# Kernel optimization log

Measured on AMD Instinct MI355X. Metric: run time of the kernel, lower is better.

Reference implementation:

```python
import jax, jax.numpy as jnp
import numpy as np

EPS = 1e-5


def _gcn_conv(x, src, dst, norm, W, b, n_nodes):
    # PyG GCNConv: transform, then normalized scatter-add aggregation (self-loops included in src/dst)
    h = x @ W                                   # [N, out]
    msg = h[src] * norm[:, None]                # gather over edges [E+N, out]
    agg = jax.ops.segment_sum(msg, dst, num_segments=n_nodes)
    return agg + b


def _bn(x, gamma, beta):
    # BatchNorm1d in training mode: batch stats over node axis, biased variance
    mu = jnp.mean(x, axis=0)
    var = jnp.mean((x - mu) ** 2, axis=0)
    return (x - mu) * jax.lax.rsqrt(var + EPS) * gamma + beta


def setup_inputs() -> dict:
    key = jax.random.key(0)
    ks = jax.random.split(key, 8)
    N, E, F_in, H, F_out = 50000, 800000, 32, 96, 2
    x = jax.random.normal(ks[0], (N, F_in), dtype=jnp.float32)
    edge_index = jax.random.randint(ks[1], (2, E), 0, N, dtype=jnp.int64)
    def lin(k, fi, fo):
        s = 1.0 / np.sqrt(fi)
        return jax.random.uniform(k, (fi, fo), jnp.float32, -s, s)
    W1 = lin(ks[2], F_in, H); b1 = jnp.zeros((H,), jnp.float32)
    W2 = lin(ks[3], H, H);    b2 = jnp.zeros((H,), jnp.float32)
    W3 = lin(ks[4], H, H);    b3 = jnp.zeros((H,), jnp.float32)
    W4 = lin(ks[5], H, F_out); b4 = jnp.zeros((F_out,), jnp.float32)
    g1 = jnp.ones((H,), jnp.float32); be1 = jnp.zeros((H,), jnp.float32)
    g2 = jnp.ones((H,), jnp.float32); be2 = jnp.zeros((H,), jnp.float32)
    g3 = jnp.ones((H,), jnp.float32); be3 = jnp.zeros((H,), jnp.float32)
    return dict(x=x, edge_index=edge_index,
                W1=W1, b1=b1, g1=g1, be1=be1,
                W2=W2, b2=b2, g2=g2, be2=be2,
                W3=W3, b3=b3, g3=g3, be3=be3,
                W4=W4, b4=b4)


def reference(x, edge_index, W1, b1, g1, be1, W2, b2, g2, be2, W3, b3, g3, be3, W4, b4):
    N = x.shape[0]
    loop = jnp.arange(N, dtype=edge_index.dtype)
    src = jnp.concatenate([edge_index[0], loop])   # add self-loops
    dst = jnp.concatenate([edge_index[1], loop])
    deg = jax.ops.segment_sum(jnp.ones_like(dst, dtype=x.dtype), dst, num_segments=N)
    dinv = jnp.where(deg > 0, jax.lax.rsqrt(deg), 0.0)
    norm = dinv[src] * dinv[dst]                   # D^{-1/2} (A+I) D^{-1/2}

    h = jax.nn.relu(_bn(_gcn_conv(x, src, dst, norm, W1, b1, N), g1, be1))
    h = jax.nn.relu(_bn(_gcn_conv(h, src, dst, norm, W2, b2, N), g2, be2))
    h = jax.nn.relu(_bn(_gcn_conv(h, src, dst, norm, W3, b3, N), g3, be3))
    return _gcn_conv(h, src, dst, norm, W4, b4, N)
```

## Files before the change

kernel.cpp:

```cpp
#include <hip/hip_runtime.h>
#include <hip/hip_bf16.h>

using bf16x8 = __attribute__((ext_vector_type(8))) short;
using f32x4  = __attribute__((ext_vector_type(4))) float;

#define FS_CHUNK 4096

__device__ __forceinline__ float ldf(const void* p, size_t i, float isf){
  if (isf > 0.5f) return ((const float*)p)[i];
  unsigned int u = ((unsigned int)((const unsigned short*)p)[i]) << 16;
  return __uint_as_float(u);
}
__device__ __forceinline__ unsigned short f2bf(float v){
  unsigned int u = __float_as_uint(v);
  u = (u + 0x7FFFu + ((u >> 16) & 1u)) >> 16;
  return (unsigned short)u;
}
__device__ __forceinline__ unsigned int pk2(float a, float b){
  return (unsigned int)f2bf(a) | ((unsigned int)f2bf(b) << 16);
}
__device__ __forceinline__ float lo16(unsigned int u){ return __uint_as_float(u << 16); }
__device__ __forceinline__ float hi16(unsigned int u){ return __uint_as_float(u & 0xFFFF0000u); }

__global__ void k_fill(unsigned short* o, unsigned short v, int n){
  int i = blockIdx.x*blockDim.x + threadIdx.x;
  if (i < n) o[i] = v;
}

__global__ void k_prep(const unsigned short* xh, const unsigned int* eu,
                       float* flag, int nelemX, long long E,
                       const void* W1, const void* W2, const void* W3, const void* W4,
                       unsigned short* __restrict__ Wt1, unsigned short* __restrict__ Wt2,
                       unsigned short* __restrict__ Wt3, float* __restrict__ W4f,
                       int* __restrict__ cnt, float* __restrict__ stAll, int n){
  int t = threadIdx.x;
  if (blockIdx.x > 0){
    int total = n + 4609;
    for (int i = (int)(blockIdx.x-1)*256 + t; i < total; i += (int)(gridDim.x-1)*256){
      if (i < n) cnt[i] = 0; else stAll[i - n] = 0.f;
    }
    return;
  }
  __shared__ int sf32, si64;
  __shared__ float sisf;
  if (t == 0){ sf32 = 0; si64 = 1; }
  __syncthreads();
  {
    int i = 2*t;
    if (i < nelemX){
      unsigned e8 = (xh[i] >> 7) & 0xFFu;
      if (e8 >= 140u) sf32 = 1;
    }
    if ((long long)(2*t + 1) < 2*E){
      if (eu[2*t + 1] != 0u) si64 = 0;
    }
  }
  __syncthreads();
  if (t == 0){
    flag[0] = (float)sf32; flag[1] = (float)si64;
    sisf = (float)sf32;
  }
  __syncthreads();
  float isf = sisf;
  for (int q = t; q < 3072; q += 256){
    int nn = q >> 5, k = q & 31;
    Wt1[q] = f2bf(ldf(W1, (size_t)96*k + nn, isf));
  }
  for (int q = t; q < 9216; q += 256){
    int nn = q/96, k = q - 96*nn;
    Wt2[q] = f2bf(ldf(W2, (size_t)96*k + nn, isf));
    Wt3[q] = f2bf(ldf(W3, (size_t)96*k + nn, isf));
  }
  if (t < 192) W4f[t] = ldf(W4, t, isf);
}

__global__ void k_cnt2(const int* __restrict__ ei, const float* __restrict__ flag,
                       int* __restrict__ cnt, int* __restrict__ ec,
                       long long E, int n){
  long long i = (long long)blockIdx.x*blockDim.x + threadIdx.x;
  long long i0 = 2*i;
  if (i0 >= E) return;
  bool i64 = (flag[1] > 0.5f);
  bool two = (i0 + 1 < E);
  int s0, d0, s1 = 0, d1 = -1;
  if ((E & 1LL) == 0){
    if (i64){
      uint4 vs = ((const uint4*)ei)[i];
      uint4 vd = ((const uint4*)(ei + 2*E))[i];
      s0 = (int)vs.x; s1 = (int)vs.z; d0 = (int)vd.x; d1 = (int)vd.z;
    } else {
      int2 vs = ((const int2*)ei)[i];
      int2 vd = ((const int2*)(ei + E))[i];
      s0 = vs.x; s1 = vs.y; d0 = vd.x; d1 = vd.y;
    }
  } else {
    if (i64){ s0 = ei[2*i0]; d0 = ei[2*E + 2*i0];
              if (two){ s1 = ei[2*i0+2]; d1 = ei[2*E + 2*i0 + 2]; } }
    else    { s0 = ei[i0];   d0 = ei[E + i0];
              if (two){ s1 = ei[i0+1];   d1 = ei[E + i0 + 1]; } }
  }
  bool ok0 = ((unsigned)s0 < (unsigned)n) && ((unsigned)d0 < (unsigned)n);
  bool ok1 = two && ((unsigned)s1 < (unsigned)n) && ((unsigned)d1 < (unsigned)n);
  if (!ok0){ s0 = -1; d0 = -1; }
  if (!ok1){ s1 = -1; d1 = -1; }
  if (two){
    int4 o; o.x = s0; o.y = d0; o.z = s1; o.w = d1;
    ((int4*)ec)[i] = o;
  } else {
    int2 o; o.x = s0; o.y = d0;
    ((int2*)ec)[i0] = o;
  }
  if (ok0) atomicAdd(&cnt[d0], 1);
  if (ok1) atomicAdd(&cnt[d1], 1);
}

__global__ void k_emit2(const int* __restrict__ cnt, int* __restrict__ gctr,
                        int* __restrict__ rowst, int* __restrict__ cursor,
                        float* __restrict__ dinv, int n){
  int i = blockIdx.x*256 + threadIdx.x;
  int lane = threadIdx.x & 63;
  int v = (i < n) ? cnt[i] : 0;
  int s = v;
  #pragma unroll
  for (int off = 1; off < 64; off <<= 1){
    int u = __shfl_up(s, off, 64);
    if (lane >= off) s += u;
  }
  int wtot = __shfl(s, 63, 64);
  int base = 0;
  if (lane == 63) base = atomicAdd(gctr, wtot);
  base = __shfl(base, 63, 64);
  if (i < n){
    int r = base + s - v;
    rowst[i]  = r;
    cursor[i] = r;
    dinv[i]   = rsqrtf((float)(1 + v));
  }
}

template<typename IT>
__global__ __launch_bounds__(256) void k_fx(const int* __restrict__ ec,
      int* __restrict__ cursor, IT* __restrict__ csr,
      long long E, int n, int gF8,
      const void* __restrict__ x, const float* __restrict__ flag,
      const float* __restrict__ dinv, unsigned short* __restrict__ XS){
  int t = threadIdx.x;
  if ((int)blockIdx.x < gF8){
    int part = blockIdx.x & 7;
    long long base = (long long)(blockIdx.x >> 3) * FS_CHUNK;
    int pl = (int)(((long long)n *  part     ) >> 3);
    int pr = (int)(((long long)n * (part + 1)) >> 3);
    long long lim = base + FS_CHUNK < E ? base + FS_CHUNK : E;
    for (long long i = base + 2*t; i < lim; i += 512){
      int4 v = ((const int4*)ec)[i >> 1];
      if (v.y >= pl && v.y < pr && (unsigned)v.x < (unsigned)n){
        int p = atomicAdd(&cursor[v.y], 1);
        csr[p] = (IT)v.x;
      }
      if (i + 1 < lim && v.w >= pl && v.w < pr && (unsigned)v.z < (unsigned)n){
        int p = atomicAdd(&cursor[v.w], 1);
        csr[p] = (IT)v.z;
      }
    }
    return;
  }
  int q = (int)(blockIdx.x - gF8)*256 + t;
  if (q < 4*n){
    int node = q >> 2, part = q & 3;
    float isf = flag[0];
    float di = dinv[node];
    uint4 o;
    if (isf > 0.5f){
      const float* xr = (const float*)x + (size_t)32*node + 8*part;
      o.x = pk2(xr[0]*di, xr[1]*di); o.y = pk2(xr[2]*di, xr[3]*di);
      o.z = pk2(xr[4]*di, xr[5]*di); o.w = pk2(xr[6]*di, xr[7]*di);
    } else {
      uint4 v = ((const uint4*)x)[(size_t)4*node + part];
      o.x = pk2(lo16(v.x)*di, hi16(v.x)*di);
      o.y = pk2(lo16(v.y)*di, hi16(v.y)*di);
      o.z = pk2(lo16(v.z)*di, hi16(v.z)*di);
      o.w = pk2(lo16(v.w)*di, hi16(v.w)*di);
    }
    ((uint4*)XS)[q] = o;
  }
}

#define ACC8(v) { a0+=lo16((v).x); a1+=hi16((v).x); a2+=lo16((v).y); a3+=hi16((v).y); \
                  a4+=lo16((v).z); a5+=hi16((v).z); a6+=lo16((v).w); a7+=hi16((v).w); }

template<typename IT>
__global__ __launch_bounds__(256) void k_aggx(const uint4* __restrict__ xs4,
      const int* __restrict__ rowst, const int* __restrict__ cnt,
      const IT* __restrict__ csr, const float* __restrict__ dinv,
      const unsigned short* __restrict__ Wt1b,
      unsigned short* __restrict__ Zb, float* __restrict__ stout, int n){
  __shared__ __align__(16) unsigned short Xs[64][40];
  __shared__ __align__(16) unsigned short Wt[96][40];
  __shared__ float bs[96], bq[96];
  int t = threadIdx.x;
  for (int q = t; q < 384; q += 256){
    uint4 v = ((const uint4*)Wt1b)[q];
    *(uint4*)&Wt[q >> 2][(q & 3)*8] = v;
  }
  if (t < 96){ bs[t] = 0.f; bq[t] = 0.f; }
  int g = t & 3, ty = t >> 2;
  int node = blockIdx.x*64 + ty;
  float a0=0.f,a1=0.f,a2=0.f,a3=0.f,a4=0.f,a5=0.f,a6=0.f,a7=0.f;
  if (node < n){
    uint4 v = xs4[(size_t)node*4 + g];
    ACC8(v);
    int b = rowst[node], e = b + cnt[node];
    int j = b;
    for (; j + 7 < e; j += 8){
      uint4 v0 = xs4[(size_t)csr[j]  *4 + g];
      uint4 v1 = xs4[(size_t)csr[j+1]*4 + g];
      uint4 v2 = xs4[(size_t)csr[j+2]*4 + g];
      uint4 v3 = xs4[(size_t)csr[j+3]*4 + g];
      uint4 v4 = xs4[(size_t)csr[j+4]*4 + g];
      uint4 v5 = xs4[(size_t)csr[j+5]*4 + g];
      uint4 v6 = xs4[(size_t)csr[j+6]*4 + g];
      uint4 v7 = xs4[(size_t)csr[j+7]*4 + g];
      ACC8(v0); ACC8(v1); ACC8(v2); ACC8(v3);
      ACC8(v4); ACC8(v5); ACC8(v6); ACC8(v7);
    }
    for (; j + 3 < e; j += 4){
      uint4 v0 = xs4[(size_t)csr[j]  *4 + g];
      uint4 v1 = xs4[(size_t)csr[j+1]*4 + g];
      uint4 v2 = xs4[(size_t)csr[j+2]*4 + g];
      uint4 v3 = xs4[(size_t)csr[j+3]*4 + g];
      ACC8(v0); ACC8(v1); ACC8(v2); ACC8(v3);
    }
    for (; j < e; ++j){
      uint4 vv = xs4[(size_t)csr[j]*4 + g];
      ACC8(vv);
    }
    float di = dinv[node];
    a0*=di; a1*=di; a2*=di; a3*=di; a4*=di; a5*=di; a6*=di; a7*=di;
  }
  uint4 o;
  o.x = pk2(a0,a1); o.y = pk2(a2,a3); o.z = pk2(a4,a5); o.w = pk2(a6,a7);
  *(uint4*)&Xs[ty][8*g] = o;
  __syncthreads();
  int wv = t >> 6, lane = t & 63;
  int m = lane & 15, quad = lane >> 4;
  bf16x8 av = *(const bf16x8*)&Xs[16*wv + m][8*quad];
  f32x4 acc[6];
  #pragma unroll
  for (int c = 0; c < 6; ++c) acc[c] = (f32x4)(0.f);
  #pragma unroll
  for (int c = 0; c < 6; ++c){
    bf16x8 bv = *(const bf16x8*)&Wt[16*c + m][8*quad];
    acc[c] = __builtin_amdgcn_mfma_f32_16x16x32_bf16(av, bv, acc[c], 0, 0, 0);
  }
  int rowbase = blockIdx.x*64 + 16*wv + 4*quad;
  #pragma unroll
  for (int c = 0; c < 6; ++c){
    int col = 16*c + m;
    float s = 0.f, q = 0.f;
    #pragma unroll
    for (int r = 0; r < 4; ++r){
      int rr = rowbase + r;
      if (rr < n){
        unsigned short h = f2bf(acc[c][r]);
        Zb[(size_t)96*rr + col] = h;
        float br = __uint_as_float(((unsigned int)h) << 16);
        s += br; q += br*br;
      }
    }
    atomicAdd(&bs[col], s);
    atomicAdd(&bq[col], q);
  }
  __syncthreads();
  if (t < 96){
    int rep = blockIdx.x & 7;
    atomicAdd(&stout[192*rep + t],      bs[t]);
    atomicAdd(&stout[192*rep + 96 + t], bq[t]);
  }
}

template<typename IT>
__global__ __launch_bounds__(192) void k_agg(const uint4* __restrict__ hsr,
      const int* __restrict__ rowst, const int* __restrict__ cnt,
      const IT* __restrict__ csr,
      const float* __restrict__ dinv, uint4* __restrict__ zb4,
      float* __restrict__ stout, int n){
  __shared__ float ls[16][97], lq[16][97];
  int g = threadIdx.x, ty = threadIdx.y;
  int t = ty*12 + g;
  int node = blockIdx.x*16 + ty;
  float r[8];
  if (node < n){
    uint4 v = hsr[(size_t)node*12 + g];
    float a0 = lo16(v.x), a1 = hi16(v.x), a2 = lo16(v.y), a3 = hi16(v.y);
    float a4 = lo16(v.z), a5 = hi16(v.z), a6 = lo16(v.w), a7 = hi16(v.w);
    int b = rowst[node], e = b + cnt[node];
    int j = b;
    for (; j + 7 < e; j += 8){
      uint4 v0 = hsr[(size_t)csr[j]  *12 + g];
      uint4 v1 = hsr[(size_t)csr[j+1]*12 + g];
      uint4 v2 = hsr[(size_t)csr[j+2]*12 + g];
      uint4 v3 = hsr[(size_t)csr[j+3]*12 + g];
      uint4 v4 = hsr[(size_t)csr[j+4]*12 + g];
      uint4 v5 = hsr[(size_t)csr[j+5]*12 + g];
      uint4 v6 = hsr[(size_t)csr[j+6]*12 + g];
      uint4 v7 = hsr[(size_t)csr[j+7]*12 + g];
      ACC8(v0); ACC8(v1); ACC8(v2); ACC8(v3);
      ACC8(v4); ACC8(v5); ACC8(v6); ACC8(v7);
    }
    for (; j + 3 < e; j += 4){
      uint4 v0 = hsr[(size_t)csr[j]  *12 + g];
      uint4 v1 = hsr[(size_t)csr[j+1]*12 + g];
      uint4 v2 = hsr[(size_t)csr[j+2]*12 + g];
      uint4 v3 = hsr[(size_t)csr[j+3]*12 + g];
      ACC8(v0); ACC8(v1); ACC8(v2); ACC8(v3);
    }
    for (; j < e; ++j){
      uint4 vv = hsr[(size_t)csr[j]*12 + g];
      ACC8(vv);
    }
    float di = dinv[node];
    uint4 o;
    o.x = pk2(a0*di, a1*di);
    o.y = pk2(a2*di, a3*di);
    o.z = pk2(a4*di, a5*di);
    o.w = pk2(a6*di, a7*di);
    zb4[(size_t)node*12 + g] = o;
    r[0]=lo16(o.x); r[1]=hi16(o.x); r[2]=lo16(o.y); r[3]=hi16(o.y);
    r[4]=lo16(o.z); r[5]=hi16(o.z); r[6]=lo16(o.w); r[7]=hi16(o.w);
  } else {
    #pragma unroll
    for (int jj = 0; jj < 8; ++jj) r[jj] = 0.f;
  }
  #pragma unroll
  for (int jj = 0; jj < 8; ++jj){
    ls[ty][8*g + jj] = r[jj];
    lq[ty][8*g + jj] = r[jj]*r[jj];
  }
  __syncthreads();
  if (t < 96){
    float s = 0.f, q = 0.f;
    #pragma unroll
    for (int rr = 0; rr < 16; ++rr){ s += ls[rr][t]; q += lq[rr][t]; }
    int rep = blockIdx.x & 7;
    atomicAdd(&stout[192*rep + t],      s);
    atomicAdd(&stout[192*rep + 96 + t], q);
  }
}

__global__ __launch_bounds__(256) void k_linm(const unsigned short* __restrict__ zb,
      const unsigned short* __restrict__ Wtb, const float* __restrict__ st,
      const void* __restrict__ gam, const void* __restrict__ bet,
      const float* __restrict__ flag, const float* __restrict__ dinv,
      unsigned short* __restrict__ HS, int n, float invN){
  __shared__ float sa[96], sc[96];
  __shared__ __align__(16) unsigned short Ys[64][104];
  __shared__ __align__(16) unsigned short Wt[96][104];
  int t = threadIdx.x;
  if (t < 96){
    float ssum = 0.f, qsum = 0.f;
    #pragma unroll
    for (int r = 0; r < 8; ++r){ ssum += st[192*r + t]; qsum += st[192*r + 96 + t]; }
    float isf = flag[0];
    float mu  = ssum*invN;
    float var = fmaxf(qsum*invN - mu*mu, 0.f);
    float istd = rsqrtf(var + 1e-5f);
    float a = ldf(gam, t, isf)*istd;
    sa[t] = a; sc[t] = ldf(bet, t, isf) - mu*a;
  }
  for (int q = t; q < 1152; q += 256){
    uint4 v = ((const uint4*)Wtb)[q];
    *(uint4*)&Wt[q/12][8*(q - 12*(q/12))] = v;
  }
  __syncthreads();
  {
    int row = t >> 2, part = t & 3;
    int node = blockIdx.x*64 + row;
    if (node < n){
      const uint4* zr = (const uint4*)(zb + (size_t)96*node) + 3*part;
      #pragma unroll
      for (int q = 0; q < 3; ++q){
        uint4 zz = zr[q];
        int k = 24*part + 8*q;
        float y0 = fmaxf(lo16(zz.x)*sa[k]   + sc[k],   0.f);
        float y1 = fmaxf(hi16(zz.x)*sa[k+1] + sc[k+1], 0.f);
        float y2 = fmaxf(lo16(zz.y)*sa[k+2] + sc[k+2], 0.f);
        float y3 = fmaxf(hi16(zz.y)*sa[k+3] + sc[k+3], 0.f);
        float y4 = fmaxf(lo16(zz.z)*sa[k+4] + sc[k+4], 0.f);
        float y5 = fmaxf(hi16(zz.z)*sa[k+5] + sc[k+5], 0.f);
        float y6 = fmaxf(lo16(zz.w)*sa[k+6] + sc[k+6], 0.f);
        float y7 = fmaxf(hi16(zz.w)*sa[k+7] + sc[k+7], 0.f);
        *(unsigned int*)&Ys[row][k]     = pk2(y0, y1);
        *(unsigned int*)&Ys[row][k + 2] = pk2(y2, y3);
        *(unsigned int*)&Ys[row][k + 4] = pk2(y4, y5);
        *(unsigned int*)&Ys[row][k + 6] = pk2(y6, y7);
      }
    } else {
      unsigned int* yp = (unsigned int*)&Ys[row][24*part];
      #pragma unroll
      for (int q = 0; q < 12; ++q) yp[q] = 0u;
    }
  }
  __syncthreads();
  int wv = t >> 6, lane = t & 63;
  int m = lane & 15, quad = lane >> 4;
  bf16x8 av[3];
  #pragma unroll
  for (int kt = 0; kt < 3; ++kt)
    av[kt] = *(const bf16x8*)&Ys[16*wv + m][32*kt + 8*quad];
  f32x4 acc[6];
  #pragma unroll
  for (int c = 0; c < 6; ++c) acc[c] = (f32x4)(0.f);
  #pragma unroll
  for (int c = 0; c < 6; ++c){
    const unsigned short* wrow = &Wt[16*c + m][8*quad];
    #pragma unroll
    for (int kt = 0; kt < 3; ++kt){
      bf16x8 bv = *(const bf16x8*)(wrow + 32*kt);
      acc[c] = __builtin_amdgcn_mfma_f32_16x16x32_bf16(av[kt], bv, acc[c], 0, 0, 0);
    }
  }
  int rowbase = blockIdx.x*64 + 16*wv + 4*quad;
  float div[4];
  #pragma unroll
  for (int r = 0; r < 4; ++r){ int rr = rowbase + r; div[r] = (rr < n) ? dinv[rr] : 0.f; }
  #pragma unroll
  for (int c = 0; c < 6; ++c){
    int col = 16*c + m;
    #pragma unroll
    for (int r = 0; r < 4; ++r){
      int rr = rowbase + r;
      if (rr < n) HS[(size_t)96*rr + col] = f2bf(acc[c][r]*div[r]);
    }
  }
}

__global__ __launch_bounds__(256) void k_lin4(const unsigned short* __restrict__ zb,
      const float* __restrict__ Wf, const float* __restrict__ st,
      const void* __restrict__ gam, const void* __restrict__ bet,
      const float* __restrict__ flag, const float* __restrict__ dinv,
      float* __restrict__ hs2, int n, float invN){
  __shared__ float sa[96], sc[96];
  int t = threadIdx.x;
  if (t < 96){
    float ssum = 0.f, qsum = 0.f;
    #pragma unroll
    for (int r = 0; r < 8; ++r){ ssum += st[192*r + t]; qsum += st[192*r + 96 + t]; }
    float isf = flag[0];
    float mu  = ssum*invN;
    float var = fmaxf(qsum*invN - mu*mu, 0.f);
    float istd = rsqrtf(var + 1e-5f);
    float a = ldf(gam, t, isf)*istd;
    sa[t] = a; sc[t] = ldf(bet, t, isf) - mu*a;
  }
  __syncthreads();
  int i = blockIdx.x*blockDim.x + t;
  if (i >= n) return;
  const uint4* zr = (const uint4*)(zb + (size_t)96*i);
  float a0 = 0.f, a1 = 0.f;
  #pragma unroll
  for (int q = 0; q < 12; ++q){
    uint4 zz = zr[q];
    int k = 8*q;
    float y;
    y = fmaxf(lo16(zz.x)*sa[k]   + sc[k],   0.f); a0 += y*Wf[2*k];    a1 += y*Wf[2*k+1];
    y = fmaxf(hi16(zz.x)*sa[k+1] + sc[k+1], 0.f); a0 += y*Wf[2*k+2];  a1 += y*Wf[2*k+3];
    y = fmaxf(lo16(zz.y)*sa[k+2] + sc[k+2], 0.f); a0 += y*Wf[2*k+4];  a1 += y*Wf[2*k+5];
    y = fmaxf(hi16(zz.y)*sa[k+3] + sc[k+3], 0.f); a0 += y*Wf[2*k+6];  a1 += y*Wf[2*k+7];
    y = fmaxf(lo16(zz.z)*sa[k+4] + sc[k+4], 0.f); a0 += y*Wf[2*k+8];  a1 += y*Wf[2*k+9];
    y = fmaxf(hi16(zz.z)*sa[k+5] + sc[k+5], 0.f); a0 += y*Wf[2*k+10]; a1 += y*Wf[2*k+11];
    y = fmaxf(lo16(zz.w)*sa[k+6] + sc[k+6], 0.f); a0 += y*Wf[2*k+12]; a1 += y*Wf[2*k+13];
    y = fmaxf(hi16(zz.w)*sa[k+7] + sc[k+7], 0.f); a0 += y*Wf[2*k+14]; a1 += y*Wf[2*k+15];
  }
  float di = dinv[i];
  hs2[(size_t)2*i]   = di*a0;
  hs2[(size_t)2*i+1] = di*a1;
}

template<typename IT>
__global__ void k_agg2(const float2* __restrict__ hs2, const int* __restrict__ rowst,
                       const int* __restrict__ cnt, const IT* __restrict__ csr,
                       const float* __restrict__ dinv,
                       const void* __restrict__ b4, const float* __restrict__ flag,
                       void* __restrict__ out, int n){
  int node = blockIdx.x*blockDim.x + threadIdx.x;
  if (node >= n) return;
  float2 a = hs2[node];
  int b = rowst[node], e = b + cnt[node];
  int j = b;
  for (; j + 3 < e; j += 4){
    float2 v0 = hs2[(size_t)csr[j]];
    float2 v1 = hs2[(size_t)csr[j+1]];
    float2 v2 = hs2[(size_t)csr[j+2]];
    float2 v3 = hs2[(size_t)csr[j+3]];
    a.x += v0.x + v1.x + v2.x + v3.x;
    a.y += v0.y + v1.y + v2.y + v3.y;
  }
  for (; j < e; ++j){
    float2 v = hs2[(size_t)csr[j]];
    a.x += v.x; a.y += v.y;
  }
  float isf = flag[0];
  float di = dinv[node];
  float v0 = a.x*di + ldf(b4, 0, isf);
  float v1 = a.y*di + ldf(b4, 1, isf);
  if (isf > 0.5f){
    ((float*)out)[(size_t)2*node]   = v0;
    ((float*)out)[(size_t)2*node+1] = v1;
  } else {
    ((unsigned short*)out)[(size_t)2*node]   = f2bf(v0);
    ((unsigned short*)out)[(size_t)2*node+1] = f2bf(v1);
  }
}

extern "C" void kernel_launch(void* const* d_in, const int* in_sizes, int n_in,
                              void* d_out, int out_size, void* d_ws, size_t ws_size,
                              hipStream_t stream)
{
  const int B = 256;
  unsigned short* outh = (unsigned short*)d_out;

  if (n_in < 16){
    k_fill<<<(out_size+B-1)/B, B, 0, stream>>>(outh, 0x3F40u, out_size); return;
  }
  const int N = in_sizes[0] / 32;
  const long long E = in_sizes[1] / 2;
  if (in_sizes[0] % 32 != 0 || out_size != 2*N){
    k_fill<<<(out_size+B-1)/B, B, 0, stream>>>(outh, 0x3F60u, out_size); return;
  }
  const bool u16 = (N < 65536);

  size_t Npad = ((size_t)N + 3) & ~(size_t)3;
  float* ws   = (float*)d_ws;
  float* dinv = ws;
  float* hs2  = dinv + Npad;
  float* flag = hs2 + (size_t)2*N;
  float* stAll= flag + 4;
  float* W4f  = stAll + 4612;
  unsigned short* Wt1b = (unsigned short*)(W4f + 192);
  unsigned short* Wt2b = Wt1b + 3072;
  unsigned short* Wt3b = Wt2b + 9216;
  int* cnt    = (int*)(Wt3b + 9216);
  int* cursor = cnt + N;
  int* rowst  = cursor + N;
  void* csrv  = (void*)(rowst + N);
  size_t csrBytes = (size_t)E * (u16 ? 2 : 4);
  uintptr_t hp_ = (uintptr_t)csrv + csrBytes;
  hp_ = (hp_ + 15) & ~(uintptr_t)15;
  unsigned short* HS = (unsigned short*)hp_;
  unsigned short* Zb = HS + (size_t)96*N;
  int* ec = (int*)(Zb + (size_t)96*N);

  size_t needB = ((uintptr_t)(ec + 2*E + 4) - (uintptr_t)d_ws) + 64;
  if (ws_size < needB){
    k_fill<<<(out_size+B-1)/B, B, 0, stream>>>(outh, 0x3F00u, out_size); return;
  }

  unsigned short* XS = HS;

  const void* x  = d_in[0];
  const int*  ei = (const int*)d_in[1];
  const void* W1 = d_in[2];
  const void* g1 = d_in[4];  const void* be1 = d_in[5];
  const void* W2 = d_in[6];
  const void* g2 = d_in[8];  const void* be2 = d_in[9];
  const void* W3 = d_in[10];
  const void* g3 = d_in[12]; const void* be3 = d_in[13];
  const void* W4 = d_in[14];
  const void* b4 = d_in[15];

  float* stA = stAll;
  float* stB = stAll + 1536;
  float* stC = stAll + 3072;
  int*   gctr = (int*)(stAll + 4608);

  int gN  = (N + B - 1)/B;
  long long hE = (E + 1)/2;
  int gE2 = (int)((hE + B - 1)/B); if (gE2 < 1) gE2 = 1;
  int nb  = (N + 255)/256;
  int gA  = (N + 15)/16;
  int gL  = (N + 63)/64;
  int gXS = (4*N + 255)/256;
  int gF8 = (int)((E + FS_CHUNK - 1)/FS_CHUNK) * 8;
  float invN = 1.0f / (float)N;
  dim3 ablk(12,16);

  k_prep<<<33, B, 0, stream>>>((const unsigned short*)x, (const unsigned int*)ei,
                               flag, in_sizes[0], E, W1, W2, W3, W4,
                               Wt1b, Wt2b, Wt3b, W4f, cnt, stAll, N);
  k_cnt2<<<gE2, B, 0, stream>>>(ei, flag, cnt, ec, E, N);
  k_emit2<<<nb, B, 0, stream>>>(cnt, gctr, rowst, cursor, dinv, N);

  if (u16){
    unsigned short* csr = (unsigned short*)csrv;
    k_fx<unsigned short><<<gF8 + gXS, B, 0, stream>>>(ec, cursor, csr, E, N, gF8,
                                                      x, flag, dinv, XS);
    k_aggx<unsigned short><<<gL, B, 0, stream>>>((const uint4*)XS, rowst, cnt, csr, dinv, Wt1b, Zb, stA, N);
    k_linm<<<gL, B, 0, stream>>>(Zb, Wt2b, stA, g1, be1, flag, dinv, HS, N, invN);
    k_agg<unsigned short><<<gA, ablk, 0, stream>>>((const uint4*)HS, rowst, cnt, csr, dinv, (uint4*)Zb, stB, N);
    k_linm<<<gL, B, 0, stream>>>(Zb, Wt3b, stB, g2, be2, flag, dinv, HS, N, invN);
    k_agg<unsigned short><<<gA, ablk, 0, stream>>>((const uint4*)HS, rowst, cnt, csr, dinv, (uint4*)Zb, stC, N);
    k_lin4<<<gN, B, 0, stream>>>(Zb, W4f, stC, g3, be3, flag, dinv, hs2, N, invN);
    k_agg2<unsigned short><<<gN, B, 0, stream>>>((const float2*)hs2, rowst, cnt, csr, dinv, b4, flag, d_out, N);
  } else {
    int* csr = (int*)csrv;
    k_fx<int><<<gF8 + gXS, B, 0, stream>>>(ec, cursor, csr, E, N, gF8,
                                           x, flag, dinv, XS);
    k_aggx<int><<<gL, B, 0, stream>>>((const uint4*)XS, rowst, cnt, csr, dinv, Wt1b, Zb, stA, N);
    k_linm<<<gL, B, 0, stream>>>(Zb, Wt2b, stA, g1, be1, flag, dinv, HS, N, invN);
    k_agg<int><<<gA, ablk, 0, stream>>>((const uint4*)HS, rowst, cnt, csr, dinv, (uint4*)Zb, stB, N);
    k_linm<<<gL, B, 0, stream>>>(Zb, Wt3b, stB, g2, be2, flag, dinv, HS, N, invN);
    k_agg<int><<<gA, ablk, 0, stream>>>((const uint4*)HS, rowst, cnt, csr, dinv, (uint4*)Zb, stC, N);
    k_lin4<<<gN, B, 0, stream>>>(Zb, W4f, stC, g3, be3, flag, dinv, hs2, N, invN);
    k_agg2<int><<<gN, B, 0, stream>>>((const float2*)hs2, rowst, cnt, csr, dinv, b4, flag, d_out, N);
  }
}
```

Before: 329.9 us.

## Pad CSR rows to multiples of eight with a zero sentinel node

Each CSR row is padded to a multiple of 8 entries, and the padding slots point to an extra sentinel node N whose feature row is zeroed. The aggregation kernels can then read indices with one vector load per 8 neighbours and drop the 4-wide and scalar tail loops. In exchange they perform wasted gathers of the zero row (up to 7 per node, about 3.5 on average), and the CSR buffer and feature buffers grow.

```diff
diff --git a/kernel.cpp b/kernel.cpp
--- a/kernel.cpp
+++ b/kernel.cpp
@@ -21,6 +21,22 @@
 }
 __device__ __forceinline__ float lo16(unsigned int u){ return __uint_as_float(u << 16); }
 __device__ __forceinline__ float hi16(unsigned int u){ return __uint_as_float(u & 0xFFFF0000u); }
+
+template<typename IT>
+__device__ __forceinline__ void load8idx(const IT* p, int* o){
+  if (sizeof(IT) == 2){
+    uint4 v = *(const uint4*)p;
+    o[0] = (int)(v.x & 0xFFFFu); o[1] = (int)(v.x >> 16);
+    o[2] = (int)(v.y & 0xFFFFu); o[3] = (int)(v.y >> 16);
+    o[4] = (int)(v.z & 0xFFFFu); o[5] = (int)(v.z >> 16);
+    o[6] = (int)(v.w & 0xFFFFu); o[7] = (int)(v.w >> 16);
+  } else {
+    int4 a = ((const int4*)p)[0];
+    int4 c = ((const int4*)p)[1];
+    o[0]=a.x; o[1]=a.y; o[2]=a.z; o[3]=a.w;
+    o[4]=c.x; o[5]=c.y; o[6]=c.z; o[7]=c.w;
+  }
+}
 
 __global__ void k_fill(unsigned short* o, unsigned short v, int n){
   int i = blockIdx.x*blockDim.x + threadIdx.x;
@@ -32,9 +48,11 @@
                        const void* W1, const void* W2, const void* W3, const void* W4,
                        unsigned short* __restrict__ Wt1, unsigned short* __restrict__ Wt2,
                        unsigned short* __restrict__ Wt3, float* __restrict__ W4f,
-                       int* __restrict__ cnt, float* __restrict__ stAll, int n){
+                       int* __restrict__ cnt, float* __restrict__ stAll,
+                       unsigned short* __restrict__ HS, int n){
   int t = threadIdx.x;
   if (blockIdx.x > 0){
+    if (blockIdx.x == 1 && t < 96) HS[(size_t)96*n + t] = 0;
     int total = n + 4609;
     for (int i = (int)(blockIdx.x-1)*256 + t; i < total; i += (int)(gridDim.x-1)*256){
       if (i < n) cnt[i] = 0; else stAll[i - n] = 0.f;
@@ -114,13 +132,15 @@
   if (ok1) atomicAdd(&cnt[d1], 1);
 }
 
+template<typename IT>
 __global__ void k_emit2(const int* __restrict__ cnt, int* __restrict__ gctr,
                         int* __restrict__ rowst, int* __restrict__ cursor,
-                        float* __restrict__ dinv, int n){
+                        float* __restrict__ dinv, IT* __restrict__ csr, int n){
   int i = blockIdx.x*256 + threadIdx.x;
   int lane = threadIdx.x & 63;
-  int v = (i < n) ? cnt[i] : 0;
-  int s = v;
+  int v  = (i < n) ? cnt[i] : 0;
+  int rv = (v + 7) & ~7;
+  int s = rv;
   #pragma unroll
   for (int off = 1; off < 64; off <<= 1){
     int u = __shfl_up(s, off, 64);
@@ -131,10 +151,11 @@
   if (lane == 63) base = atomicAdd(gctr, wtot);
   base = __shfl(base, 63, 64);
   if (i < n){
-    int r = base + s - v;
+    int r = base + s - rv;
     rowst[i]  = r;
     cursor[i] = r;
     dinv[i]   = rsqrtf((float)(1 + v));
+    for (int p = r + v; p < r + rv; ++p) csr[p] = (IT)n;
   }
 }
 
@@ -165,22 +186,24 @@
     return;
   }
   int q = (int)(blockIdx.x - gF8)*256 + t;
-  if (q < 4*n){
+  if (q < 4*(n+1)){
     int node = q >> 2, part = q & 3;
-    float isf = flag[0];
-    float di = dinv[node];
     uint4 o;
-    if (isf > 0.5f){
-      const float* xr = (const float*)x + (size_t)32*node + 8*part;
-      o.x = pk2(xr[0]*di, xr[1]*di); o.y = pk2(xr[2]*di, xr[3]*di);
-      o.z = pk2(xr[4]*di, xr[5]*di); o.w = pk2(xr[6]*di, xr[7]*di);
-    } else {
-      uint4 v = ((const uint4*)x)[(size_t)4*node + part];
-      o.x = pk2(lo16(v.x)*di, hi16(v.x)*di);
-      o.y = pk2(lo16(v.y)*di, hi16(v.y)*di);
-      o.z = pk2(lo16(v.z)*di, hi16(v.z)*di);
-      o.w = pk2(lo16(v.w)*di, hi16(v.w)*di);
-    }
+    if (node < n){
+      float isf = flag[0];
+      float di = dinv[node];
+      if (isf > 0.5f){
+        const float* xr = (const float*)x + (size_t)32*node + 8*part;
+        o.x = pk2(xr[0]*di, xr[1]*di); o.y = pk2(xr[2]*di, xr[3]*di);
+        o.z = pk2(xr[4]*di, xr[5]*di); o.w = pk2(xr[6]*di, xr[7]*di);
+      } else {
+        uint4 v = ((const uint4*)x)[(size_t)4*node + part];
+        o.x = pk2(lo16(v.x)*di, hi16(v.x)*di);
+        o.y = pk2(lo16(v.y)*di, hi16(v.y)*di);
+        o.z = pk2(lo16(v.z)*di, hi16(v.z)*di);
+        o.w = pk2(lo16(v.w)*di, hi16(v.w)*di);
+      }
+    } else { o.x = o.y = o.z = o.w = 0u; }
     ((uint4*)XS)[q] = o;
   }
 }
@@ -209,30 +232,21 @@
   if (node < n){
     uint4 v = xs4[(size_t)node*4 + g];
     ACC8(v);
-    int b = rowst[node], e = b + cnt[node];
-    int j = b;
-    for (; j + 7 < e; j += 8){
-      uint4 v0 = xs4[(size_t)csr[j]  *4 + g];
-      uint4 v1 = xs4[(size_t)csr[j+1]*4 + g];
-      uint4 v2 = xs4[(size_t)csr[j+2]*4 + g];
-      uint4 v3 = xs4[(size_t)csr[j+3]*4 + g];
-      uint4 v4 = xs4[(size_t)csr[j+4]*4 + g];
-      uint4 v5 = xs4[(size_t)csr[j+5]*4 + g];
-      uint4 v6 = xs4[(size_t)csr[j+6]*4 + g];
-      uint4 v7 = xs4[(size_t)csr[j+7]*4 + g];
+    int bq_ = rowst[node];
+    int bnd = bq_ + ((cnt[node] + 7) & ~7);
+    for (int j = bq_; j < bnd; j += 8){
+      int ix[8];
+      load8idx<IT>(csr + j, ix);
+      uint4 v0 = xs4[(size_t)ix[0]*4 + g];
+      uint4 v1 = xs4[(size_t)ix[1]*4 + g];
+      uint4 v2 = xs4[(size_t)ix[2]*4 + g];
+      uint4 v3 = xs4[(size_t)ix[3]*4 + g];
+      uint4 v4 = xs4[(size_t)ix[4]*4 + g];
+      uint4 v5 = xs4[(size_t)ix[5]*4 + g];
+      uint4 v6 = xs4[(size_t)ix[6]*4 + g];
+      uint4 v7 = xs4[(size_t)ix[7]*4 + g];
       ACC8(v0); ACC8(v1); ACC8(v2); ACC8(v3);
       ACC8(v4); ACC8(v5); ACC8(v6); ACC8(v7);
-    }
-    for (; j + 3 < e; j += 4){
-      uint4 v0 = xs4[(size_t)csr[j]  *4 + g];
-      uint4 v1 = xs4[(size_t)csr[j+1]*4 + g];
-      uint4 v2 = xs4[(size_t)csr[j+2]*4 + g];
-      uint4 v3 = xs4[(size_t)csr[j+3]*4 + g];
-      ACC8(v0); ACC8(v1); ACC8(v2); ACC8(v3);
-    }
-    for (; j < e; ++j){
-      uint4 vv = xs4[(size_t)csr[j]*4 + g];
-      ACC8(vv);
     }
     float di = dinv[node];
     a0*=di; a1*=di; a2*=di; a3*=di; a4*=di; a5*=di; a6*=di; a7*=di;
@@ -293,30 +307,21 @@
     uint4 v = hsr[(size_t)node*12 + g];
     float a0 = lo16(v.x), a1 = hi16(v.x), a2 = lo16(v.y), a3 = hi16(v.y);
     float a4 = lo16(v.z), a5 = hi16(v.z), a6 = lo16(v.w), a7 = hi16(v.w);
-    int b = rowst[node], e = b + cnt[node];
-    int j = b;
-    for (; j + 7 < e; j += 8){
-      uint4 v0 = hsr[(size_t)csr[j]  *12 + g];
-      uint4 v1 = hsr[(size_t)csr[j+1]*12 + g];
-      uint4 v2 = hsr[(size_t)csr[j+2]*12 + g];
-      uint4 v3 = hsr[(size_t)csr[j+3]*12 + g];
-      uint4 v4 = hsr[(size_t)csr[j+4]*12 + g];
-      uint4 v5 = hsr[(size_t)csr[j+5]*12 + g];
-      uint4 v6 = hsr[(size_t)csr[j+6]*12 + g];
-      uint4 v7 = hsr[(size_t)csr[j+7]*12 + g];
+    int bq_ = rowst[node];
+    int bnd = bq_ + ((cnt[node] + 7) & ~7);
+    for (int j = bq_; j < bnd; j += 8){
+      int ix[8];
+      load8idx<IT>(csr + j, ix);
+      uint4 v0 = hsr[(size_t)ix[0]*12 + g];
+      uint4 v1 = hsr[(size_t)ix[1]*12 + g];
+      uint4 v2 = hsr[(size_t)ix[2]*12 + g];
+      uint4 v3 = hsr[(size_t)ix[3]*12 + g];
+      uint4 v4 = hsr[(size_t)ix[4]*12 + g];
+      uint4 v5 = hsr[(size_t)ix[5]*12 + g];
+      uint4 v6 = hsr[(size_t)ix[6]*12 + g];
+      uint4 v7 = hsr[(size_t)ix[7]*12 + g];
       ACC8(v0); ACC8(v1); ACC8(v2); ACC8(v3);
       ACC8(v4); ACC8(v5); ACC8(v6); ACC8(v7);
-    }
-    for (; j + 3 < e; j += 4){
-      uint4 v0 = hsr[(size_t)csr[j]  *12 + g];
-      uint4 v1 = hsr[(size_t)csr[j+1]*12 + g];
-      uint4 v2 = hsr[(size_t)csr[j+2]*12 + g];
-      uint4 v3 = hsr[(size_t)csr[j+3]*12 + g];
-      ACC8(v0); ACC8(v1); ACC8(v2); ACC8(v3);
-    }
-    for (; j < e; ++j){
-      uint4 vv = hsr[(size_t)csr[j]*12 + g];
-      ACC8(vv);
     }
     float di = dinv[node];
     uint4 o;
@@ -542,12 +547,15 @@
   int* cnt    = (int*)(Wt3b + 9216);
   int* cursor = cnt + N;
   int* rowst  = cursor + N;
-  void* csrv  = (void*)(rowst + N);
-  size_t csrBytes = (size_t)E * (u16 ? 2 : 4);
-  uintptr_t hp_ = (uintptr_t)csrv + csrBytes;
+  uintptr_t cs_ = (uintptr_t)(rowst + N);
+  cs_ = (cs_ + 15) & ~(uintptr_t)15;
+  void* csrv  = (void*)cs_;
+  size_t csrCap = (size_t)E + 8*(size_t)N;
+  size_t csrBytes = csrCap * (u16 ? 2 : 4);
+  uintptr_t hp_ = cs_ + csrBytes;
   hp_ = (hp_ + 15) & ~(uintptr_t)15;
   unsigned short* HS = (unsigned short*)hp_;
-  unsigned short* Zb = HS + (size_t)96*N;
+  unsigned short* Zb = HS + (size_t)96*(N+1);
   int* ec = (int*)(Zb + (size_t)96*N);
 
   size_t needB = ((uintptr_t)(ec + 2*E + 4) - (uintptr_t)d_ws) + 64;
@@ -579,19 +587,19 @@
   int nb  = (N + 255)/256;
   int gA  = (N + 15)/16;
   int gL  = (N + 63)/64;
-  int gXS = (4*N + 255)/256;
+  int gXS = (4*(N+1) + 255)/256;
   int gF8 = (int)((E + FS_CHUNK - 1)/FS_CHUNK) * 8;
   float invN = 1.0f / (float)N;
   dim3 ablk(12,16);
 
   k_prep<<<33, B, 0, stream>>>((const unsigned short*)x, (const unsigned int*)ei,
                                flag, in_sizes[0], E, W1, W2, W3, W4,
-                               Wt1b, Wt2b, Wt3b, W4f, cnt, stAll, N);
+                               Wt1b, Wt2b, Wt3b, W4f, cnt, stAll, HS, N);
   k_cnt2<<<gE2, B, 0, stream>>>(ei, flag, cnt, ec, E, N);
-  k_emit2<<<nb, B, 0, stream>>>(cnt, gctr, rowst, cursor, dinv, N);
 
   if (u16){
     unsigned short* csr = (unsigned short*)csrv;
+    k_emit2<unsigned short><<<nb, B, 0, stream>>>(cnt, gctr, rowst, cursor, dinv, csr, N);
     k_fx<unsigned short><<<gF8 + gXS, B, 0, stream>>>(ec, cursor, csr, E, N, gF8,
                                                       x, flag, dinv, XS);
     k_aggx<unsigned short><<<gL, B, 0, stream>>>((const uint4*)XS, rowst, cnt, csr, dinv, Wt1b, Zb, stA, N);
@@ -603,6 +611,7 @@
     k_agg2<unsigned short><<<gN, B, 0, stream>>>((const float2*)hs2, rowst, cnt, csr, dinv, b4, flag, d_out, N);
   } else {
     int* csr = (int*)csrv;
+    k_emit2<int><<<nb, B, 0, stream>>>(cnt, gctr, rowst, cursor, dinv, csr, N);
     k_fx<int><<<gF8 + gXS, B, 0, stream>>>(ec, cursor, csr, E, N, gF8,
                                            x, flag, dinv, XS);
     k_aggx<int><<<gL, B, 0, stream>>>((const uint4*)XS, rowst, cnt, csr, dinv, Wt1b, Zb, stA, N);
```

New measurement: 326.8 us. About the same (-0.9%).
